# Kernel optimization log

Measured on AMD Instinct MI355X. Metric: run time of the kernel, lower is better.

Reference implementation:

```python
import jax, jax.numpy as jnp
import numpy as np

N, E = 20000, 320000
IN_DIM = 18            # 2 (pos) + k_feat=16
P = 32                 # in_proj_out
H1, D1 = 8, 32         # gat1 heads, head_dim (out_dim = P*heads = 256)
OUT = P * H1           # 256
BD, H2, D2 = 256, 8, 32  # bottleneck dim / heads / head_dim
NID = 1000             # num_real_ids
NEG_SLOPE = 0.2


def _ln(x, g, b, eps=1e-5):
    mu = x.mean(-1, keepdims=True)
    v = ((x - mu) ** 2).mean(-1, keepdims=True)
    return (x - mu) * jax.lax.rsqrt(v + eps) * g + b


def _segment_softmax(score, dst, n):
    # score: [E, H], softmax over edges sharing the same dst node
    m = jax.ops.segment_max(score, dst, num_segments=n)
    e = jnp.exp(score - m[dst])
    s = jax.ops.segment_sum(e, dst, num_segments=n)
    return e / (s[dst] + 1e-16)


def _gatv2(x, src, dst, ea, Wl, Wr, We, att, bias, n, h, d):
    # GATv2 (PyG semantics): e_ij = att . leaky_relu(Wl x_j + Wr x_i + We e_ij)
    xl = (x @ Wl).reshape(n, h, d)           # source transform
    xr = (x @ Wr).reshape(n, h, d)           # target transform
    xe = (ea @ We).reshape(-1, h, d)         # edge embedding [E,h,d]
    f = jax.nn.leaky_relu(xl[src] + xr[dst] + xe, NEG_SLOPE)  # [E,h,d]
    score = jnp.einsum('ehd,hd->eh', f, att)                   # [E,h]
    alpha = _segment_softmax(score, dst, n)                    # [E,h]
    out = jax.ops.segment_sum(alpha[:, :, None] * xl[src], dst, num_segments=n)
    return out.reshape(n, h * d) + bias


def setup_inputs() -> dict:
    key = jax.random.key(0)
    ks = jax.random.split(key, 20)
    s = 0.05
    rn = lambda k, shape: (jax.random.normal(k, shape, jnp.float32) * s)
    return {
        'x_gnn': jax.random.normal(ks[0], (N, IN_DIM), jnp.float32),
        'edge_index': jax.random.randint(ks[1], (2, E), 0, N),
        'edge_attr': jax.random.uniform(ks[2], (E, 1), dtype=jnp.float32),
        'W_in': rn(ks[3], (IN_DIM, P)), 'b_in': jnp.zeros((P,), jnp.float32),
        'Wl1': rn(ks[4], (P, OUT)), 'Wr1': rn(ks[5], (P, OUT)),
        'We1': rn(ks[6], (1, OUT)), 'att1': rn(ks[7], (H1, D1)),
        'bg1': jnp.zeros((OUT,), jnp.float32),
        'ln1_g': jnp.ones((OUT,), jnp.float32), 'ln1_b': jnp.zeros((OUT,), jnp.float32),
        'W_down': rn(ks[8], (OUT, BD)),
        'lnd_g': jnp.ones((BD,), jnp.float32), 'lnd_b': jnp.zeros((BD,), jnp.float32),
        'Wl2': rn(ks[9], (BD, BD)), 'Wr2': rn(ks[10], (BD, BD)),
        'We2': rn(ks[11], (1, BD)), 'att2': rn(ks[12], (H2, D2)),
        'bg2': jnp.zeros((BD,), jnp.float32),
        'ln2_g': jnp.ones((BD,), jnp.float32), 'ln2_b': jnp.zeros((BD,), jnp.float32),
        'W_up': rn(ks[13], (BD, OUT)),
        'lnu_g': jnp.ones((OUT,), jnp.float32), 'lnu_b': jnp.zeros((OUT,), jnp.float32),
        'W_cls': rn(ks[14], (OUT, NID)), 'b_cls': jnp.zeros((NID,), jnp.float32),
    }


def reference(x_gnn, edge_index, edge_attr, W_in, b_in,
              Wl1, Wr1, We1, att1, bg1, ln1_g, ln1_b,
              W_down, lnd_g, lnd_b,
              Wl2, Wr2, We2, att2, bg2, ln2_g, ln2_b,
              W_up, lnu_g, lnu_b, W_cls, b_cls):
    src, dst = edge_index[0], edge_index[1]
    h0 = x_gnn @ W_in + b_in
    # GATv2Block 1: conv + LN (no residual, 32 -> 256)
    g1 = _gatv2(h0, src, dst, edge_attr, Wl1, Wr1, We1, att1, bg1, N, H1, D1)
    h1 = _ln(g1, ln1_g, ln1_b)
    # bottleneck branch
    z = _ln(h1 @ W_down, lnd_g, lnd_b)
    # GATv2Block 2: conv + residual + LN (256 -> 256)
    g2 = _gatv2(z, src, dst, edge_attr, Wl2, Wr2, We2, att2, bg2, N, H2, D2)
    z2 = _ln(g2 + z, ln2_g, ln2_b)
    h2 = z2 @ W_up                       # up projection (dropout is identity in eval)
    h = _ln(h1 + h2, lnu_g, lnu_b)
    logits = h @ W_cls + b_cls
    return (logits, h)
```

## Files before the change

kernel.cpp:

```cpp
#include <hip/hip_runtime.h>
#include <math.h>

#define N_NODES 20000
#define N_EDGES 320000

typedef __attribute__((ext_vector_type(8))) __bf16 bf16x8;
typedef __attribute__((ext_vector_type(8))) unsigned short ushort8;
typedef __attribute__((ext_vector_type(4))) float floatx4;

__device__ __forceinline__ unsigned short f2b(float f) {
    unsigned int u = __float_as_uint(f);
    unsigned int r = (u + 0x7fffu + ((u >> 16) & 1u)) >> 16;
    return (unsigned short)r;
}
__device__ __forceinline__ float b2f(unsigned short u) {
    return __uint_as_float(((unsigned int)u) << 16);
}

__global__ void k_prep(const float* __restrict__ x, const float* __restrict__ Wi,
                       const float* __restrict__ bi, unsigned short* __restrict__ h0,
                       const int* __restrict__ dst, int* __restrict__ cnt,
                       const float* __restrict__ Wl1, const float* __restrict__ Wr1,
                       const float* __restrict__ Wdn, const float* __restrict__ Wl2,
                       const float* __restrict__ Wr2, const float* __restrict__ Wup,
                       const float* __restrict__ Wcl,
                       unsigned short* __restrict__ o1, unsigned short* __restrict__ o2,
                       unsigned short* __restrict__ o3, unsigned short* __restrict__ o4,
                       unsigned short* __restrict__ o5, unsigned short* __restrict__ o6,
                       unsigned short* __restrict__ o7) {
    int t = blockIdx.x * blockDim.x + threadIdx.x;
    if (t < 640000) {
        int n = t >> 5, p = t & 31;
        float acc = bi[p];
        const float* xr = x + n * 18;
#pragma unroll
        for (int k = 0; k < 18; k++) acc = fmaf(xr[k], Wi[k * 32 + p], acc);
        h0[t] = f2b(acc);
        return;
    }
    if (t < 960000) {
        atomicAdd(cnt + dst[t - 640000], 1);
        return;
    }
    int u = t - 960000;
    const float* W; unsigned short* O; int Nd, K, idx;
    if (u < 8192)        { W = Wl1; O = o1; Nd = 256;  K = 32;  idx = u; }
    else if (u < 16384)  { W = Wr1; O = o2; Nd = 256;  K = 32;  idx = u - 8192; }
    else if (u < 81920)  { W = Wdn; O = o3; Nd = 256;  K = 256; idx = u - 16384; }
    else if (u < 147456) { W = Wl2; O = o4; Nd = 256;  K = 256; idx = u - 81920; }
    else if (u < 212992) { W = Wr2; O = o5; Nd = 256;  K = 256; idx = u - 147456; }
    else if (u < 278528) { W = Wup; O = o6; Nd = 256;  K = 256; idx = u - 212992; }
    else if (u < 540672) { W = Wcl; O = o7; Nd = 1000; K = 256; idx = u - 278528; }
    else return;
    int n = idx / K, k = idx % K;
    float v = (n < Nd) ? W[(size_t)k * Nd + n] : 0.f;
    O[idx] = f2b(v);
}

__global__ __launch_bounds__(256) void k_gemm_bf16(
    const unsigned short* __restrict__ A, const unsigned short* __restrict__ Bt,
    float* __restrict__ Cf, unsigned short* __restrict__ Cb,
    const float* __restrict__ bias, int M, int N, int K) {
    __shared__ unsigned short As[8 * 64 * 8];
    __shared__ unsigned short Bs[8 * 64 * 8];
    int tid = threadIdx.x;
    int wave = tid >> 6, lane = tid & 63;
    int wr = wave >> 1, wc = wave & 1;
    int row0 = blockIdx.x * 128, col0 = blockIdx.y * 128;
    floatx4 zero4 = {0.f, 0.f, 0.f, 0.f};
    floatx4 acc[4][4];
#pragma unroll
    for (int i = 0; i < 4; i++)
#pragma unroll
        for (int j = 0; j < 4; j++) acc[i][j] = zero4;
    for (int kb = 0; kb < K; kb += 32) {
#pragma unroll
        for (int q = 0; q < 2; q++) {
            int c = tid * 2 + q;
            int row = c >> 2, koff = (c & 3) * 8;
            int lp = (row & 15) + 16 * (koff >> 3);
            int mt = row >> 4;
            ushort8 va = {0, 0, 0, 0, 0, 0, 0, 0};
            if (row0 + row < M)
                va = *(const ushort8*)(A + (size_t)(row0 + row) * K + kb + koff);
            *(ushort8*)(As + (mt * 64 + lp) * 8) = va;
            ushort8 vb = {0, 0, 0, 0, 0, 0, 0, 0};
            if (col0 + row < N)
                vb = *(const ushort8*)(Bt + (size_t)(col0 + row) * K + kb + koff);
            *(ushort8*)(Bs + (mt * 64 + lp) * 8) = vb;
        }
        __syncthreads();
        bf16x8 af[4], bfr[4];
#pragma unroll
        for (int i = 0; i < 4; i++)
            af[i] = *(const bf16x8*)(As + ((wr * 4 + i) * 64 + lane) * 8);
#pragma unroll
        for (int j = 0; j < 4; j++)
            bfr[j] = *(const bf16x8*)(Bs + ((wc * 4 + j) * 64 + lane) * 8);
#pragma unroll
        for (int i = 0; i < 4; i++)
#pragma unroll
            for (int j = 0; j < 4; j++)
                acc[i][j] = __builtin_amdgcn_mfma_f32_16x16x32_bf16(
                    af[i], bfr[j], acc[i][j], 0, 0, 0);
        __syncthreads();
    }
    int quad = lane >> 4, nl = lane & 15;
#pragma unroll
    for (int i = 0; i < 4; i++) {
#pragma unroll
        for (int j = 0; j < 4; j++) {
            int col = col0 + wc * 64 + j * 16 + nl;
            if (col >= N) continue;
            float bv = bias ? bias[col] : 0.f;
#pragma unroll
            for (int r = 0; r < 4; r++) {
                int rr = row0 + wr * 64 + i * 16 + quad * 4 + r;
                if (rr >= M) continue;
                float v = acc[i][j][r] + bv;
                if (Cf) Cf[(size_t)rr * N + col] = v;
                else Cb[(size_t)rr * N + col] = f2b(v);
            }
        }
    }
}

__global__ __launch_bounds__(512) void k_gemm_reg(
    const unsigned short* __restrict__ A,
    const unsigned short* __restrict__ Bt,
    int Ncols, int ldC,
    const float* __restrict__ bias,
    const float* __restrict__ res,
    const float* __restrict__ g, const float* __restrict__ b,
    float* __restrict__ outf, unsigned short* __restrict__ outb) {
    __shared__ unsigned short As[16 * 256];
    __shared__ float red[8][16][2];
    int tid = threadIdx.x, lane = tid & 63, wave = tid >> 6;
    int nl = lane & 15, quad = lane >> 4;
    int row0 = blockIdx.x * 16;
    int cbase = blockIdx.y * 256 + wave * 32;

    {
        int r = tid >> 5, c = tid & 31;
        ushort8 v = *(const ushort8*)(A + (size_t)(row0 + r) * 256 + c * 8);
        *(ushort8*)(As + r * 256 + ((c ^ (r & 7)) << 3)) = v;
    }
    bf16x8 breg[2][8];
    const unsigned short* bptr = Bt + (size_t)(cbase + nl) * 256 + quad * 8;
#pragma unroll
    for (int j = 0; j < 2; j++)
#pragma unroll
        for (int kb = 0; kb < 8; kb++)
            breg[j][kb] = *(const bf16x8*)(bptr + j * 16 * 256 + kb * 32);
    __syncthreads();

    floatx4 zero4 = {0.f, 0.f, 0.f, 0.f};
    floatx4 acc[2];
    acc[0] = zero4; acc[1] = zero4;
#pragma unroll
    for (int kb = 0; kb < 8; kb++) {
        int kq = kb * 4 + quad;
        bf16x8 a = *(const bf16x8*)(As + nl * 256 + (((kq ^ (nl & 7))) << 3));
        acc[0] = __builtin_amdgcn_mfma_f32_16x16x32_bf16(a, breg[0][kb], acc[0], 0, 0, 0);
        acc[1] = __builtin_amdgcn_mfma_f32_16x16x32_bf16(a, breg[1][kb], acc[1], 0, 0, 0);
    }

    if (g == nullptr) {
#pragma unroll
        for (int j = 0; j < 2; j++) {
            int col = cbase + j * 16 + nl;
            if (col >= Ncols) continue;
            float bv = bias ? bias[col] : 0.f;
#pragma unroll
            for (int r = 0; r < 4; r++) {
                int rr = row0 + quad * 4 + r;
                float v = acc[j][r] + bv;
                if (outf) outf[(size_t)rr * ldC + col] = v;
                if (outb) outb[(size_t)rr * ldC + col] = f2b(v);
            }
        }
        return;
    }

    if (res) {
#pragma unroll
        for (int j = 0; j < 2; j++) {
            int col = cbase + j * 16 + nl;
#pragma unroll
            for (int r = 0; r < 4; r++)
                acc[j][r] += res[(size_t)(row0 + quad * 4 + r) * 256 + col];
        }
    }
#pragma unroll
    for (int r = 0; r < 4; r++) {
        float s = acc[0][r] + acc[1][r];
        float q = fmaf(acc[0][r], acc[0][r], acc[1][r] * acc[1][r]);
        s += __shfl_xor(s, 1, 64); q += __shfl_xor(q, 1, 64);
        s += __shfl_xor(s, 2, 64); q += __shfl_xor(q, 2, 64);
        s += __shfl_xor(s, 4, 64); q += __shfl_xor(q, 4, 64);
        s += __shfl_xor(s, 8, 64); q += __shfl_xor(q, 8, 64);
        if (nl == 0) {
            red[wave][quad * 4 + r][0] = s;
            red[wave][quad * 4 + r][1] = q;
        }
    }
    __syncthreads();
    float mean_[4], rstd_[4];
#pragma unroll
    for (int r = 0; r < 4; r++) {
        int row = quad * 4 + r;
        float s = 0.f, q = 0.f;
#pragma unroll
        for (int w = 0; w < 8; w++) { s += red[w][row][0]; q += red[w][row][1]; }
        float mean = s * (1.0f / 256.0f);
        float var = q * (1.0f / 256.0f) - mean * mean;
        mean_[r] = mean;
        rstd_[r] = 1.0f / sqrtf(var + 1e-5f);
    }
#pragma unroll
    for (int j = 0; j < 2; j++) {
        int col = cbase + j * 16 + nl;
        float gv = g[col], bvv = b[col];
#pragma unroll
        for (int r = 0; r < 4; r++) {
            int rr = row0 + quad * 4 + r;
            float o = (acc[j][r] - mean_[r]) * rstd_[r] * gv + bvv;
            if (outf) outf[(size_t)rr * 256 + col] = o;
            if (outb) outb[(size_t)rr * 256 + col] = f2b(o);
        }
    }
}

__global__ __launch_bounds__(1024) void k_scan(const int* __restrict__ cnt,
                                               int* __restrict__ rowptr,
                                               int* __restrict__ wp, int n) {
    __shared__ int tsum[1024];
    int t = threadIdx.x;
    const int chunk = 20;
    int i0 = t * chunk;
    int local[chunk];
    int s = 0;
#pragma unroll
    for (int j = 0; j < chunk; j++) {
        int i = i0 + j;
        int v = (i < n) ? cnt[i] : 0;
        local[j] = s;
        s += v;
    }
    tsum[t] = s;
    __syncthreads();
    for (int off = 1; off < 1024; off <<= 1) {
        int other = (t >= off) ? tsum[t - off] : 0;
        __syncthreads();
        tsum[t] += other;
        __syncthreads();
    }
    int base = (t > 0) ? tsum[t - 1] : 0;
#pragma unroll
    for (int j = 0; j < chunk; j++) {
        int i = i0 + j;
        if (i < n) {
            int ex = base + local[j];
            rowptr[i] = ex;
            wp[i] = ex;
        }
    }
    if (t == 1023) rowptr[n] = tsum[1023];
}

__global__ void k_fill(const int* __restrict__ src, const int* __restrict__ dst,
                       const float* __restrict__ ea, int* __restrict__ wp,
                       int* __restrict__ srcs, float* __restrict__ eas) {
    int e = blockIdx.x * blockDim.x + threadIdx.x;
    if (e >= N_EDGES) return;
    int p = atomicAdd(wp + dst[e], 1);
    srcs[p] = src[e];
    eas[p] = ea[e];
}

__global__ __launch_bounds__(256) void k_gat_ln(
    const int* __restrict__ rowptr, const int* __restrict__ srcs,
    const float* __restrict__ eas, const unsigned short* __restrict__ xlr,
    const float* __restrict__ We, const float* __restrict__ att,
    const float* __restrict__ vbias, const float* __restrict__ res,
    const float* __restrict__ g, const float* __restrict__ b,
    float* __restrict__ outf, unsigned short* __restrict__ outb) {
    int node = blockIdx.x * 4 + (threadIdx.x >> 6);
    if (node >= N_NODES) return;
    int lane = threadIdx.x & 63;
    int beg = rowptr[node], end = rowptr[node + 1];
    float4 wv = ((const float4*)We)[lane];
    float4 av = ((const float4*)att)[lane];
    ushort4 xru = ((const ushort4*)(xlr + (size_t)node * 512 + 256))[lane];
    float4 rv = make_float4(b2f(xru.x), b2f(xru.y), b2f(xru.z), b2f(xru.w));
    float m = -3.0e38f, l = 0.f;
    float4 acc = make_float4(0.f, 0.f, 0.f, 0.f);
    if (beg < end) {
        int last = end - 1;
        int i1 = (beg + 1 < end) ? beg + 1 : last;
        int i2 = (beg + 2 < end) ? beg + 2 : last;
        int i3 = (beg + 3 < end) ? beg + 3 : last;
        int i4 = (beg + 4 < end) ? beg + 4 : last;
        int i5 = (beg + 5 < end) ? beg + 5 : last;
        int i6 = (beg + 6 < end) ? beg + 6 : last;
        int i7 = (beg + 7 < end) ? beg + 7 : last;
        int s0a = srcs[beg], s0b = srcs[i1];
        int s1a = srcs[i2],  s1b = srcs[i3];
        int s2a = srcs[i4],  s2b = srcs[i5];
        int s3a = srcs[i6],  s3b = srcs[i7];
        float a0a = eas[beg], a0b = eas[i1];
        float a1a = eas[i2],  a1b = eas[i3];
        float a2a = eas[i4],  a2b = eas[i5];
        float a3a = eas[i6],  a3b = eas[i7];
        ushort4 x0a = ((const ushort4*)(xlr + (size_t)s0a * 512))[lane];
        ushort4 x0b = ((const ushort4*)(xlr + (size_t)s0b * 512))[lane];
        ushort4 x1a = ((const ushort4*)(xlr + (size_t)s1a * 512))[lane];
        ushort4 x1b = ((const ushort4*)(xlr + (size_t)s1b * 512))[lane];
        ushort4 x2a = ((const ushort4*)(xlr + (size_t)s2a * 512))[lane];
        ushort4 x2b = ((const ushort4*)(xlr + (size_t)s2b * 512))[lane];
        for (int i = beg; i < end; i += 2) {
            int j8 = (i + 8 < end) ? i + 8 : last;
            int j9 = (i + 9 < end) ? i + 9 : last;
            int s4a = srcs[j8], s4b = srcs[j9];
            float a4a = eas[j8], a4b = eas[j9];
            ushort4 x3a = ((const ushort4*)(xlr + (size_t)s3a * 512))[lane];
            ushort4 x3b = ((const ushort4*)(xlr + (size_t)s3b * 512))[lane];
            float4 lva = make_float4(b2f(x0a.x), b2f(x0a.y), b2f(x0a.z), b2f(x0a.w));
            float4 lvb = make_float4(b2f(x0b.x), b2f(x0b.y), b2f(x0b.z), b2f(x0b.w));
            float f, pa = 0.f, pb = 0.f;
            f = lva.x + rv.x + a0a * wv.x; f = fmaxf(f, 0.2f * f); pa = fmaf(f, av.x, pa);
            f = lva.y + rv.y + a0a * wv.y; f = fmaxf(f, 0.2f * f); pa = fmaf(f, av.y, pa);
            f = lva.z + rv.z + a0a * wv.z; f = fmaxf(f, 0.2f * f); pa = fmaf(f, av.z, pa);
            f = lva.w + rv.w + a0a * wv.w; f = fmaxf(f, 0.2f * f); pa = fmaf(f, av.w, pa);
            f = lvb.x + rv.x + a0b * wv.x; f = fmaxf(f, 0.2f * f); pb = fmaf(f, av.x, pb);
            f = lvb.y + rv.y + a0b * wv.y; f = fmaxf(f, 0.2f * f); pb = fmaf(f, av.y, pb);
            f = lvb.z + rv.z + a0b * wv.z; f = fmaxf(f, 0.2f * f); pb = fmaf(f, av.z, pb);
            f = lvb.w + rv.w + a0b * wv.w; f = fmaxf(f, 0.2f * f); pb = fmaf(f, av.w, pb);
            pa += __shfl_xor(pa, 1, 64);
            pa += __shfl_xor(pa, 2, 64);
            pa += __shfl_xor(pa, 4, 64);
            pb += __shfl_xor(pb, 1, 64);
            pb += __shfl_xor(pb, 2, 64);
            pb += __shfl_xor(pb, 4, 64);
            if (i + 1 >= end) pb = -3.0e38f;
            float mnew = fmaxf(fmaxf(m, pa), pb);
            float scale = __expf(m - mnew);
            float wa = __expf(pa - mnew);
            float wb = __expf(pb - mnew);
            acc.x = fmaf(acc.x, scale, fmaf(wa, lva.x, wb * lvb.x));
            acc.y = fmaf(acc.y, scale, fmaf(wa, lva.y, wb * lvb.y));
            acc.z = fmaf(acc.z, scale, fmaf(wa, lva.z, wb * lvb.z));
            acc.w = fmaf(acc.w, scale, fmaf(wa, lva.w, wb * lvb.w));
            l = fmaf(l, scale, wa + wb);
            m = mnew;
            x0a = x1a; x0b = x1b; x1a = x2a; x1b = x2b; x2a = x3a; x2b = x3b;
            a0a = a1a; a0b = a1b; a1a = a2a; a1b = a2b; a2a = a3a; a2b = a3b;
            a3a = a4a; a3b = a4b; s3a = s4a; s3b = s4b;
        }
    }
    float inv = 1.0f / (l + 1e-16f);
    float4 vb4 = ((const float4*)vbias)[lane];
    float4 o = make_float4(fmaf(acc.x, inv, vb4.x), fmaf(acc.y, inv, vb4.y),
                           fmaf(acc.z, inv, vb4.z), fmaf(acc.w, inv, vb4.w));
    if (res) {
        float4 r4 = ((const float4*)(res + (size_t)node * 256))[lane];
        o.x += r4.x; o.y += r4.y; o.z += r4.z; o.w += r4.w;
    }
    float sum = o.x + o.y + o.z + o.w;
#pragma unroll
    for (int off = 32; off > 0; off >>= 1) sum += __shfl_xor(sum, off, 64);
    float mean = sum * (1.0f / 256.0f);
    float dx = o.x - mean, dy = o.y - mean, dz = o.z - mean, dw = o.w - mean;
    float sq = dx * dx + dy * dy + dz * dz + dw * dw;
#pragma unroll
    for (int off = 32; off > 0; off >>= 1) sq += __shfl_xor(sq, off, 64);
    float rstd = 1.0f / sqrtf(sq * (1.0f / 256.0f) + 1e-5f);
    float4 gg = ((const float4*)g)[lane];
    float4 bb = ((const float4*)b)[lane];
    float4 o4 = make_float4(dx * rstd * gg.x + bb.x, dy * rstd * gg.y + bb.y,
                            dz * rstd * gg.z + bb.z, dw * rstd * gg.w + bb.w);
    if (outf) ((float4*)(outf + (size_t)node * 256))[lane] = o4;
    if (outb) {
        ushort4 u;
        u.x = f2b(o4.x); u.y = f2b(o4.y); u.z = f2b(o4.z); u.w = f2b(o4.w);
        ((ushort4*)(outb + (size_t)node * 256))[lane] = u;
    }
}

extern "C" void kernel_launch(void* const* d_in, const int* in_sizes, int n_in,
                              void* d_out, int out_size, void* d_ws, size_t ws_size,
                              hipStream_t stream) {
    const float* x_gnn = (const float*)d_in[0];
    const int* ei = (const int*)d_in[1];
    const int* src = ei;
    const int* dst = ei + N_EDGES;
    const float* ea   = (const float*)d_in[2];
    const float* W_in = (const float*)d_in[3];
    const float* b_in = (const float*)d_in[4];
    const float* Wl1  = (const float*)d_in[5];
    const float* Wr1  = (const float*)d_in[6];
    const float* We1  = (const float*)d_in[7];
    const float* att1 = (const float*)d_in[8];
    const float* bg1  = (const float*)d_in[9];
    const float* ln1_g = (const float*)d_in[10];
    const float* ln1_b = (const float*)d_in[11];
    const float* W_down = (const float*)d_in[12];
    const float* lnd_g = (const float*)d_in[13];
    const float* lnd_b = (const float*)d_in[14];
    const float* Wl2  = (const float*)d_in[15];
    const float* Wr2  = (const float*)d_in[16];
    const float* We2  = (const float*)d_in[17];
    const float* att2 = (const float*)d_in[18];
    const float* bg2  = (const float*)d_in[19];
    const float* ln2_g = (const float*)d_in[20];
    const float* ln2_b = (const float*)d_in[21];
    const float* W_up = (const float*)d_in[22];
    const float* lnu_g = (const float*)d_in[23];
    const float* lnu_b = (const float*)d_in[24];
    const float* W_cls = (const float*)d_in[25];
    const float* b_cls = (const float*)d_in[26];

    float* ws = (float*)d_ws;
    float* B_agg = ws;
    float* B_h1  = B_agg + 5120000;
    float* B_z   = B_h1 + 5120000;
    unsigned short* B_xlr = (unsigned short*)(B_z + 5120000);
    unsigned short* B_actb = B_xlr + 10240000;
    unsigned short* B_h0b = B_actb + 5120000;
    unsigned short* Wt_l1 = B_h0b + 640000;
    unsigned short* Wt_r1 = Wt_l1 + 8192;
    unsigned short* Wt_down = Wt_r1 + 8192;
    unsigned short* Wt_l2 = Wt_down + 65536;
    unsigned short* Wt_r2 = Wt_l2 + 65536;
    unsigned short* Wt_up = Wt_r2 + 65536;
    unsigned short* Wt_cls = Wt_up + 65536;
    int* C_cnt = (int*)(Wt_cls + 262144);
    int* C_row = C_cnt + 20000;
    int* C_wp  = C_row + 20001;
    int* C_src = C_wp + 20000;
    float* C_ea = (float*)(C_src + 320000);

    float* out_logits = (float*)d_out;
    float* out_h = out_logits + (size_t)N_NODES * 1000;

    int gatblk = (N_NODES + 3) / 4;
    int gemmM16 = N_NODES / 16;
    dim3 gl((N_NODES + 127) / 128, 4);

    hipMemsetAsync(C_cnt, 0, (size_t)20000 * 4, stream);
    k_prep<<<5862, 256, 0, stream>>>(x_gnn, W_in, b_in, B_h0b, dst, C_cnt,
                                     Wl1, Wr1, W_down, Wl2, Wr2, W_up, W_cls,
                                     Wt_l1, Wt_r1, Wt_down, Wt_l2, Wt_r2, Wt_up, Wt_cls);
    k_scan<<<1, 1024, 0, stream>>>(C_cnt, C_row, C_wp, N_NODES);
    k_fill<<<(N_EDGES + 255) / 256, 256, 0, stream>>>(src, dst, ea, C_wp, C_src, C_ea);

    k_gemm_bf16<<<gl, 256, 0, stream>>>(B_h0b, Wt_l1, nullptr, B_xlr, nullptr, N_NODES, 512, 32);
    k_gat_ln<<<gatblk, 256, 0, stream>>>(C_row, C_src, C_ea, B_xlr, We1, att1,
                                         bg1, nullptr, ln1_g, ln1_b, B_h1, B_actb);
    k_gemm_reg<<<dim3(gemmM16, 1), 512, 0, stream>>>(
        B_actb, Wt_down, 256, 256, nullptr, nullptr, lnd_g, lnd_b, B_z, B_actb);
    k_gemm_reg<<<dim3(gemmM16, 2), 512, 0, stream>>>(
        B_actb, Wt_l2, 512, 512, nullptr, nullptr, nullptr, nullptr, nullptr, B_xlr);
    k_gat_ln<<<gatblk, 256, 0, stream>>>(C_row, C_src, C_ea, B_xlr, We2, att2,
                                         bg2, B_z, ln2_g, ln2_b, nullptr, B_actb);
    k_gemm_reg<<<dim3(gemmM16, 1), 512, 0, stream>>>(
        B_actb, Wt_up, 256, 256, nullptr, B_h1, lnu_g, lnu_b, out_h, B_actb);
    k_gemm_reg<<<dim3(gemmM16, 4), 512, 0, stream>>>(
        B_actb, Wt_cls, 1000, 1000, b_cls, nullptr, nullptr, nullptr,
        out_logits, nullptr);
}
```

Before: 478.2 us.

## Make register-B GEMM persistent with grid-stride row tiles and double-buffered A

Replaces the one-block-per-16-row-tile GEMM with a persistent grid-stride kernel. Each block loads its weight slice into registers once and reuses it across many row tiles. The next A tile is prefetched into a second LDS buffer while the current tile is computed. This is meant to cut repeated weight loads and per-block launch overhead, at the cost of fewer blocks (less parallelism), a hardcoded tile count of 1250, and an extra barrier per iteration.

New measurement: 402.4 us. -15.8%, faster.

```diff
diff --git a/kernel.cpp b/kernel.cpp
--- a/kernel.cpp
+++ b/kernel.cpp
@@ -125,7 +125,7 @@
     }
 }
 
-__global__ __launch_bounds__(512) void k_gemm_reg(
+__global__ __launch_bounds__(512) void k_gemm_stride(
     const unsigned short* __restrict__ A,
     const unsigned short* __restrict__ Bt,
     int Ncols, int ldC,
@@ -133,18 +133,15 @@
     const float* __restrict__ res,
     const float* __restrict__ g, const float* __restrict__ b,
     float* __restrict__ outf, unsigned short* __restrict__ outb) {
-    __shared__ unsigned short As[16 * 256];
+    __shared__ unsigned short As[2][16 * 256];
     __shared__ float red[8][16][2];
     int tid = threadIdx.x, lane = tid & 63, wave = tid >> 6;
     int nl = lane & 15, quad = lane >> 4;
-    int row0 = blockIdx.x * 16;
     int cbase = blockIdx.y * 256 + wave * 32;
-
-    {
-        int r = tid >> 5, c = tid & 31;
-        ushort8 v = *(const ushort8*)(A + (size_t)(row0 + r) * 256 + c * 8);
-        *(ushort8*)(As + r * 256 + ((c ^ (r & 7)) << 3)) = v;
-    }
+    int sr = tid >> 5, sc = tid & 31;
+    int swz = (sc ^ (sr & 7)) << 3;
+    int R = gridDim.x;
+
     bf16x8 breg[2][8];
     const unsigned short* bptr = Bt + (size_t)(cbase + nl) * 256 + quad * 8;
 #pragma unroll
@@ -152,82 +149,102 @@
 #pragma unroll
         for (int kb = 0; kb < 8; kb++)
             breg[j][kb] = *(const bf16x8*)(bptr + j * 16 * 256 + kb * 32);
+
+    int s = blockIdx.x;
+    {
+        ushort8 v = *(const ushort8*)(A + ((size_t)s * 16 + sr) * 256 + sc * 8);
+        *(ushort8*)(&As[0][sr * 256 + swz]) = v;
+    }
     __syncthreads();
-
-    floatx4 zero4 = {0.f, 0.f, 0.f, 0.f};
-    floatx4 acc[2];
-    acc[0] = zero4; acc[1] = zero4;
-#pragma unroll
-    for (int kb = 0; kb < 8; kb++) {
-        int kq = kb * 4 + quad;
-        bf16x8 a = *(const bf16x8*)(As + nl * 256 + (((kq ^ (nl & 7))) << 3));
-        acc[0] = __builtin_amdgcn_mfma_f32_16x16x32_bf16(a, breg[0][kb], acc[0], 0, 0, 0);
-        acc[1] = __builtin_amdgcn_mfma_f32_16x16x32_bf16(a, breg[1][kb], acc[1], 0, 0, 0);
-    }
-
-    if (g == nullptr) {
-#pragma unroll
-        for (int j = 0; j < 2; j++) {
-            int col = cbase + j * 16 + nl;
-            if (col >= Ncols) continue;
-            float bv = bias ? bias[col] : 0.f;
+    int p = 0;
+    while (s < 1250) {
+        int snext = s + R;
+        bool more = (snext < 1250);
+        ushort8 av;
+        if (more)
+            av = *(const ushort8*)(A + ((size_t)snext * 16 + sr) * 256 + sc * 8);
+
+        floatx4 acc0 = {0.f, 0.f, 0.f, 0.f};
+        floatx4 acc1 = {0.f, 0.f, 0.f, 0.f};
+#pragma unroll
+        for (int kb = 0; kb < 8; kb++) {
+            int kq = kb * 4 + quad;
+            bf16x8 a = *(const bf16x8*)(&As[p][nl * 256 + (((kq ^ (nl & 7))) << 3)]);
+            acc0 = __builtin_amdgcn_mfma_f32_16x16x32_bf16(a, breg[0][kb], acc0, 0, 0, 0);
+            acc1 = __builtin_amdgcn_mfma_f32_16x16x32_bf16(a, breg[1][kb], acc1, 0, 0, 0);
+        }
+        int row0 = s * 16;
+
+        if (g == nullptr) {
+#pragma unroll
+            for (int j = 0; j < 2; j++) {
+                int col = cbase + j * 16 + nl;
+                if (col < Ncols) {
+                    float bv = bias ? bias[col] : 0.f;
+                    floatx4 aj = j ? acc1 : acc0;
+#pragma unroll
+                    for (int r = 0; r < 4; r++) {
+                        int rr = row0 + quad * 4 + r;
+                        float v = aj[r] + bv;
+                        if (outf) outf[(size_t)rr * ldC + col] = v;
+                        if (outb) outb[(size_t)rr * ldC + col] = f2b(v);
+                    }
+                }
+            }
+        } else {
+            if (res) {
+#pragma unroll
+                for (int r = 0; r < 4; r++) {
+                    int rr = row0 + quad * 4 + r;
+                    acc0[r] += res[(size_t)rr * 256 + cbase + nl];
+                    acc1[r] += res[(size_t)rr * 256 + cbase + 16 + nl];
+                }
+            }
 #pragma unroll
             for (int r = 0; r < 4; r++) {
-                int rr = row0 + quad * 4 + r;
-                float v = acc[j][r] + bv;
-                if (outf) outf[(size_t)rr * ldC + col] = v;
-                if (outb) outb[(size_t)rr * ldC + col] = f2b(v);
-            }
-        }
-        return;
-    }
-
-    if (res) {
-#pragma unroll
-        for (int j = 0; j < 2; j++) {
-            int col = cbase + j * 16 + nl;
-#pragma unroll
-            for (int r = 0; r < 4; r++)
-                acc[j][r] += res[(size_t)(row0 + quad * 4 + r) * 256 + col];
-        }
-    }
-#pragma unroll
-    for (int r = 0; r < 4; r++) {
-        float s = acc[0][r] + acc[1][r];
-        float q = fmaf(acc[0][r], acc[0][r], acc[1][r] * acc[1][r]);
-        s += __shfl_xor(s, 1, 64); q += __shfl_xor(q, 1, 64);
-        s += __shfl_xor(s, 2, 64); q += __shfl_xor(q, 2, 64);
-        s += __shfl_xor(s, 4, 64); q += __shfl_xor(q, 4, 64);
-        s += __shfl_xor(s, 8, 64); q += __shfl_xor(q, 8, 64);
-        if (nl == 0) {
-            red[wave][quad * 4 + r][0] = s;
-            red[wave][quad * 4 + r][1] = q;
-        }
-    }
-    __syncthreads();
-    float mean_[4], rstd_[4];
-#pragma unroll
-    for (int r = 0; r < 4; r++) {
-        int row = quad * 4 + r;
-        float s = 0.f, q = 0.f;
-#pragma unroll
-        for (int w = 0; w < 8; w++) { s += red[w][row][0]; q += red[w][row][1]; }
-        float mean = s * (1.0f / 256.0f);
-        float var = q * (1.0f / 256.0f) - mean * mean;
-        mean_[r] = mean;
-        rstd_[r] = 1.0f / sqrtf(var + 1e-5f);
-    }
-#pragma unroll
-    for (int j = 0; j < 2; j++) {
-        int col = cbase + j * 16 + nl;
-        float gv = g[col], bvv = b[col];
-#pragma unroll
-        for (int r = 0; r < 4; r++) {
-            int rr = row0 + quad * 4 + r;
-            float o = (acc[j][r] - mean_[r]) * rstd_[r] * gv + bvv;
-            if (outf) outf[(size_t)rr * 256 + col] = o;
-            if (outb) outb[(size_t)rr * 256 + col] = f2b(o);
-        }
+                float su = acc0[r] + acc1[r];
+                float q = fmaf(acc0[r], acc0[r], acc1[r] * acc1[r]);
+                su += __shfl_xor(su, 1, 64); q += __shfl_xor(q, 1, 64);
+                su += __shfl_xor(su, 2, 64); q += __shfl_xor(q, 2, 64);
+                su += __shfl_xor(su, 4, 64); q += __shfl_xor(q, 4, 64);
+                su += __shfl_xor(su, 8, 64); q += __shfl_xor(q, 8, 64);
+                if (nl == 0) {
+                    red[wave][quad * 4 + r][0] = su;
+                    red[wave][quad * 4 + r][1] = q;
+                }
+            }
+            __syncthreads();
+            float mean_[4], rstd_[4];
+#pragma unroll
+            for (int r = 0; r < 4; r++) {
+                int row = quad * 4 + r;
+                float su = 0.f, q = 0.f;
+#pragma unroll
+                for (int w = 0; w < 8; w++) { su += red[w][row][0]; q += red[w][row][1]; }
+                float mean = su * (1.0f / 256.0f);
+                float var = q * (1.0f / 256.0f) - mean * mean;
+                mean_[r] = mean;
+                rstd_[r] = 1.0f / sqrtf(var + 1e-5f);
+            }
+#pragma unroll
+            for (int j = 0; j < 2; j++) {
+                int col = cbase + j * 16 + nl;
+                float gv = g[col], bvv = b[col];
+                floatx4 aj = j ? acc1 : acc0;
+#pragma unroll
+                for (int r = 0; r < 4; r++) {
+                    int rr = row0 + quad * 4 + r;
+                    float o = (aj[r] - mean_[r]) * rstd_[r] * gv + bvv;
+                    if (outf) outf[(size_t)rr * 256 + col] = o;
+                    if (outb) outb[(size_t)rr * 256 + col] = f2b(o);
+                }
+            }
+        }
+
+        if (more) *(ushort8*)(&As[p ^ 1][sr * 256 + swz]) = av;
+        __syncthreads();
+        p ^= 1;
+        s = snext;
     }
 }
 
@@ -444,7 +461,6 @@
     float* out_h = out_logits + (size_t)N_NODES * 1000;
 
     int gatblk = (N_NODES + 3) / 4;
-    int gemmM16 = N_NODES / 16;
     dim3 gl((N_NODES + 127) / 128, 4);
 
     hipMemsetAsync(C_cnt, 0, (size_t)20000 * 4, stream);
@@ -457,15 +473,15 @@
     k_gemm_bf16<<<gl, 256, 0, stream>>>(B_h0b, Wt_l1, nullptr, B_xlr, nullptr, N_NODES, 512, 32);
     k_gat_ln<<<gatblk, 256, 0, stream>>>(C_row, C_src, C_ea, B_xlr, We1, att1,
                                          bg1, nullptr, ln1_g, ln1_b, B_h1, B_actb);
-    k_gemm_reg<<<dim3(gemmM16, 1), 512, 0, stream>>>(
+    k_gemm_stride<<<dim3(512, 1), 512, 0, stream>>>(
         B_actb, Wt_down, 256, 256, nullptr, nullptr, lnd_g, lnd_b, B_z, B_actb);
-    k_gemm_reg<<<dim3(gemmM16, 2), 512, 0, stream>>>(
+    k_gemm_stride<<<dim3(256, 2), 512, 0, stream>>>(
         B_actb, Wt_l2, 512, 512, nullptr, nullptr, nullptr, nullptr, nullptr, B_xlr);
     k_gat_ln<<<gatblk, 256, 0, stream>>>(C_row, C_src, C_ea, B_xlr, We2, att2,
                                          bg2, B_z, ln2_g, ln2_b, nullptr, B_actb);
-    k_gemm_reg<<<dim3(gemmM16, 1), 512, 0, stream>>>(
+    k_gemm_stride<<<dim3(512, 1), 512, 0, stream>>>(
         B_actb, Wt_up, 256, 256, nullptr, B_h1, lnu_g, lnu_b, out_h, B_actb);
-    k_gemm_reg<<<dim3(gemmM16, 4), 512, 0, stream>>>(
+    k_gemm_stride<<<dim3(128, 4), 512, 0, stream>>>(
         B_actb, Wt_cls, 1000, 1000, b_cls, nullptr, nullptr, nullptr,
         out_logits, nullptr);
 }
```
